# Performance work log

Measured on AMD Instinct MI355X. Metric: run time of the kernel, lower is better.

Reference implementation:

```python
import jax, jax.numpy as jnp
import numpy as np

C_IN, C_OUT = 64, 32
SD, RFF = 2, 16
RF = 0.05          # receptive_field percentile
TEMP = 1.0
EPS = 1e-8
RFF_STD = 6.0


def setup_inputs() -> dict:
    key = jax.random.key(0)
    ks = jax.random.split(key, 10)
    B_, T, V, Q = 2, 4, 2048, 512
    x = jax.random.normal(ks[0], (B_, T, V, C_IN), dtype=jnp.float32)
    pos = jax.random.uniform(ks[1], (V, SD), dtype=jnp.float32)
    query_pos = jax.random.uniform(ks[2], (Q, SD), dtype=jnp.float32)
    s = 1.0 / np.sqrt(C_IN)
    W_lin = jax.random.uniform(ks[3], (C_IN, C_IN), minval=-s, maxval=s, dtype=jnp.float32)
    b_lin = jax.random.uniform(ks[4], (C_IN,), minval=-s, maxval=s, dtype=jnp.float32)
    Bmat = RFF_STD * jax.random.normal(ks[5], (SD, RFF), dtype=jnp.float32)
    s1 = 1.0 / np.sqrt(32)
    W1 = jax.random.uniform(ks[6], (32, 32), minval=-s1, maxval=s1, dtype=jnp.float32)
    b1 = jax.random.uniform(ks[7], (32,), minval=-s1, maxval=s1, dtype=jnp.float32)
    W2 = jax.random.uniform(ks[8], (C_IN * C_OUT, 32), minval=-s1, maxval=s1, dtype=jnp.float32)
    sf = np.sqrt(3.0 / C_IN)
    filt = jax.random.uniform(ks[9], (C_IN * C_OUT,), minval=-sf, maxval=sf, dtype=jnp.float32)
    bias = jnp.zeros((C_OUT,), dtype=jnp.float32)
    return {"x": x, "pos": pos, "query_pos": query_pos, "W_lin": W_lin, "b_lin": b_lin,
            "Bmat": Bmat, "W1": W1, "b1": b1, "W2": W2, "filt": filt, "bias": bias}


def reference(x, pos, query_pos, W_lin, b_lin, Bmat, W1, b1, W2, filt, bias):
    # pairwise periodic displacement / squared distance
    dist = query_pos[:, None, :] - pos[None, :, :]            # (Q, V, 2)
    dist = (dist + 0.5) % 1.0 - 0.5                           # periodic wrap
    edist = jnp.sum(dist ** 2, axis=-1)                       # (Q, V)
    # quantile threshold -> max neighbourhood size (eager, data-dependent like torch)
    thr = jnp.quantile(edist, RF, axis=-1, keepdims=True)     # linear interpolation, as torch
    K = int(jnp.max(jnp.sum(edist <= thr, axis=-1)))
    _, ind = jax.lax.top_k(-edist, K)                         # (Q, K) nearest neighbours
    # gather per-query neighbour displacements / distances
    d_g = jnp.take_along_axis(dist, ind[..., None], axis=1)   # (Q, K, 2)
    e_g = jnp.take_along_axis(edist, ind, axis=1)[..., None]  # (Q, K, 1)
    e_g = e_g - jnp.min(e_g, axis=-2, keepdims=True)
    e_g = e_g / (jnp.max(e_g, axis=-2, keepdims=True) + EPS)
    k_dist = jax.nn.softmax(-e_g / TEMP, axis=-2)             # (Q, K, 1)
    # random Fourier features + kernel MLP
    proj = 2.0 * jnp.pi * (d_g @ Bmat)                        # (Q, K, 16)
    kfeat = jnp.concatenate([jnp.sin(proj), jnp.cos(proj)], axis=-1)  # (Q, K, 32)
    h = jax.nn.gelu(kfeat @ W1.T + b1, approximate=False)
    ker = (h @ W2.T + filt) * k_dist                          # (Q, K, C_IN*C_OUT)
    ker = ker.reshape(ker.shape[0], ker.shape[1], C_IN, C_OUT)
    # point-wise linear on features, then gather + contract
    xl = x @ W_lin.T + b_lin                                  # (B, T, V, C_IN)
    xg = xl[:, :, ind, :]                                     # (B, T, Q, K, C_IN)
    return jnp.einsum('qvcd,btqvc->btqd', ker, xg) + bias     # (B, T, Q, C_OUT)
```

## Files before the change

### kernel.cpp

```cpp
#include <hip/hip_runtime.h>

#define K_SEL 103
typedef unsigned long long ull_t;
typedef _Float16 f16x8 __attribute__((ext_vector_type(8)));
typedef float f32x4 __attribute__((ext_vector_type(4)));

__global__ __launch_bounds__(256, 4) void k12(const float* __restrict__ pos,
                                              const float* __restrict__ qpos,
                                              const float* __restrict__ Bmat,
                                              const float* __restrict__ W1,
                                              const float* __restrict__ b1,
                                              _Float16* __restrict__ Hh,
                                              int* __restrict__ indg,
                                              float* __restrict__ invtot,
                                              const float* __restrict__ x,
                                              const float* __restrict__ W,
                                              const float* __restrict__ b,
                                              _Float16* __restrict__ xlh,
                                              const float* __restrict__ W2,
                                              const float* __restrict__ filt,
                                              _Float16* __restrict__ W2th) {
    __shared__ __align__(16) unsigned char smem[30848];
    const int tid = threadIdx.x;
    const int bid = blockIdx.x;
    const int lane = tid & 63;
    const int wid = tid >> 6;

    if (bid >= 512) {
        const int bb = bid - 512;
        float* Wt = (float*)smem;
        if (tid < 132) {
            int t = bb * 132 + tid;
            int d = t & 31;
            int e = t >> 5;
            int c = e & 63;
            int j = e >> 6;
            float v = (j < 32) ? W2[(c * 32 + d) * 32 + j] : filt[c * 32 + d];
            W2th[d * 2112 + e] = (_Float16)v;
        }
        for (int t = tid; t < 4096; t += 256)
            Wt[(t & 63) * 64 + (t >> 6)] = W[t];
        __syncthreads();
        const int i = tid & 63;
        const int sub = tid >> 6;
        const float bi = b[i];
        #pragma unroll
        for (int rr = 0; rr < 2; ++rr) {
            const int r0 = bb * 32 + rr * 16 + sub * 4;
            float acc0 = bi, acc1 = bi, acc2 = bi, acc3 = bi;
            const float* xr = x + (size_t)r0 * 64;
            #pragma unroll 4
            for (int jj = 0; jj < 16; ++jj) {
                float4 v0 = *(const float4*)(xr + 0 * 64 + jj * 4);
                float4 v1 = *(const float4*)(xr + 1 * 64 + jj * 4);
                float4 v2 = *(const float4*)(xr + 2 * 64 + jj * 4);
                float4 v3 = *(const float4*)(xr + 3 * 64 + jj * 4);
                float w0 = Wt[(jj * 4 + 0) * 64 + i];
                float w1 = Wt[(jj * 4 + 1) * 64 + i];
                float w2 = Wt[(jj * 4 + 2) * 64 + i];
                float w3 = Wt[(jj * 4 + 3) * 64 + i];
                acc0 += v0.x * w0 + v0.y * w1 + v0.z * w2 + v0.w * w3;
                acc1 += v1.x * w0 + v1.y * w1 + v1.z * w2 + v1.w * w3;
                acc2 += v2.x * w0 + v2.y * w1 + v2.z * w2 + v2.w * w3;
                acc3 += v3.x * w0 + v3.y * w1 + v3.z * w2 + v3.w * w3;
            }
            xlh[(size_t)(r0 + 0) * 64 + i] = (_Float16)acc0;
            xlh[(size_t)(r0 + 1) * 64 + i] = (_Float16)acc1;
            xlh[(size_t)(r0 + 2) * 64 + i] = (_Float16)acc2;
            xlh[(size_t)(r0 + 3) * 64 + i] = (_Float16)acc3;
        }
        return;
    }

    const int q = bid;
    unsigned* ebits   = (unsigned*)(smem);
    unsigned* hist    = (unsigned*)(smem + 8192);
    _Float16* Hs      = (_Float16*)(smem + 8192);
    float*    W1s     = (float*)(smem + 24576);
    float*    b1s     = (float*)(smem + 28672);
    float*    Bm      = (float*)(smem + 28800);
    int*      sel_v   = (int*)(smem + 28928);
    float*    sel_e   = (float*)(smem + 29344);
    ull_t*    bnd     = (ull_t*)(smem + 29760);
    int*      counters= (int*)(smem + 30784);
    int*      info    = (int*)(smem + 30792);
    float*    wred    = (float*)(smem + 30800);
    float*    emax_s  = (float*)(smem + 30816);
    unsigned* wscan   = (unsigned*)(smem + 30824);

    for (int t = tid; t < 1024; t += 256) W1s[t] = W1[t];
    if (tid < 32) { b1s[tid] = b1[tid]; Bm[tid] = Bmat[tid]; }
    if (tid < 2)  counters[tid] = 0;
    for (int t = tid; t < 1024; t += 256) ((uint4*)hist)[t] = make_uint4(0, 0, 0, 0);
    const float qp0 = qpos[q * 2 + 0];
    const float qp1 = qpos[q * 2 + 1];
    __syncthreads();

    float lmin = 1e30f;
    for (int v = tid; v < 2048; v += 256) {
        float2 p = ((const float2*)pos)[v];
        float d0 = qp0 - p.x;
        float d1 = qp1 - p.y;
        d0 += 0.5f; d0 -= floorf(d0); d0 -= 0.5f;
        d1 += 0.5f; d1 -= floorf(d1); d1 -= 0.5f;
        float e = d0 * d0 + d1 * d1;
        ebits[v] = __float_as_uint(e);
        lmin = fminf(lmin, e);
        int bb2 = (int)(e * 8192.0f); bb2 = (bb2 > 4095) ? 4095 : bb2;
        atomicAdd(&hist[bb2], 1u);
    }
    #pragma unroll
    for (int off = 32; off > 0; off >>= 1)
        lmin = fminf(lmin, __shfl_xor(lmin, off, 64));
    if (lane == 0) wred[wid] = lmin;
    __syncthreads();
    const float e_min = fminf(fminf(wred[0], wred[1]), fminf(wred[2], wred[3]));

    unsigned lsum = 0;
    #pragma unroll
    for (int i = 0; i < 16; ++i) lsum += hist[tid * 16 + i];
    unsigned vq = lsum;
    #pragma unroll
    for (int off = 1; off < 64; off <<= 1) {
        unsigned n = __shfl_up(vq, off, 64);
        if (lane >= off) vq += n;
    }
    if (lane == 63) wscan[wid] = vq;
    __syncthreads();
    unsigned base = 0;
    for (int w2 = 0; w2 < wid; ++w2) base += wscan[w2];
    unsigned cum = base + vq - lsum;
    #pragma unroll
    for (int i = 0; i < 16; ++i) {
        unsigned cnt = hist[tid * 16 + i];
        if (cum <= 102u && 102u < cum + cnt) { info[0] = tid * 16 + i; info[1] = (int)cum; }
        cum += cnt;
    }
    __syncthreads();
    const int Bstar = info[0];
    const int L = info[1];
    const int need = K_SEL - L;

    {
        f16x8 z = {0, 0, 0, 0, 0, 0, 0, 0};
        for (int t = tid; t < 768; t += 256) ((f16x8*)Hs)[t] = z;
    }
    for (int v = tid; v < 2048; v += 256) {
        unsigned bb2 = ebits[v];
        float e = __uint_as_float(bb2);
        int bin = (int)(e * 8192.0f); bin = (bin > 4095) ? 4095 : bin;
        if (bin < Bstar) {
            int s2 = atomicAdd(&counters[0], 1);
            sel_v[s2] = v; sel_e[s2] = e;
        } else if (bin == Bstar) {
            int s2 = atomicAdd(&counters[1], 1);
            if (s2 < 128) bnd[s2] = (((ull_t)bb2) << 32) | (unsigned)v;
        }
    }
    __syncthreads();
    if (tid == 0) {
        int nb = counters[1]; if (nb > 128) nb = 128;
        for (int i = 1; i < nb; ++i) {
            ull_t key = bnd[i]; int j2 = i - 1;
            while (j2 >= 0 && bnd[j2] > key) { bnd[j2 + 1] = bnd[j2]; --j2; }
            bnd[j2 + 1] = key;
        }
        for (int i = 0; i < need; ++i) {
            sel_v[L + i] = (int)(unsigned)(bnd[i] & 0xffffffffull);
            sel_e[L + i] = __uint_as_float((unsigned)(bnd[i] >> 32));
        }
        emax_s[0] = __uint_as_float((unsigned)(bnd[need - 1] >> 32));
    }
    __syncthreads();

    const float denom = (emax_s[0] - e_min) + 1e-8f;
    float w = 0.0f;
    if (tid < K_SEL) {
        w = __expf(-(sel_e[tid] - e_min) / denom);
        sel_e[tid] = w;
    }
    float sw = w;
    #pragma unroll
    for (int off = 32; off > 0; off >>= 1)
        sw += __shfl_xor(sw, off, 64);
    if (lane == 0) wred[wid] = sw;
    __syncthreads();
    if (tid == 0)
        invtot[q] = 1.0f / (wred[0] + wred[1] + wred[2] + wred[3]);

    if (tid < 2 * K_SEL) {
        const int k = tid >> 1;
        const int io = (tid & 1) * 16;
        const int v = sel_v[k];
        const float wk = sel_e[k];
        float2 p = ((const float2*)pos)[v];
        float d0 = qp0 - p.x;
        float d1 = qp1 - p.y;
        d0 += 0.5f; d0 -= floorf(d0); d0 -= 0.5f;
        d1 += 0.5f; d1 -= floorf(d1); d1 -= 0.5f;
        float kf[32];
        #pragma unroll
        for (int f = 0; f < 16; ++f) {
            float t = d0 * Bm[f] + d1 * Bm[16 + f];
            float r = t - rintf(t);
            kf[f]      = __builtin_amdgcn_sinf(r);
            kf[16 + f] = __builtin_amdgcn_cosf(r);
        }
        #pragma unroll 4
        for (int i = io; i < io + 16; ++i) {
            float pre = b1s[i];
            #pragma unroll
            for (int jf = 0; jf < 32; ++jf) pre += kf[jf] * W1s[i * 32 + jf];
            float g = 0.5f * pre * (1.0f + erff(pre * 0.70710678118654752f));
            Hs[i * 128 + k] = (_Float16)(g * wk);
        }
        if (io == 0) {
            Hs[32 * 128 + k] = (_Float16)wk;
            indg[q * K_SEL + k] = v;
        }
    }
    __syncthreads();
    {
        _Float16* hq = Hh + (size_t)q * 6144;
        for (int t = tid; t < 768; t += 256)
            ((f16x8*)hq)[t] = ((const f16x8*)Hs)[t];
    }
}

__global__ __launch_bounds__(256, 4) void k3_main(const _Float16* __restrict__ xlh,
                                                  const _Float16* __restrict__ Hh,
                                                  const int* __restrict__ indg,
                                                  const _Float16* __restrict__ W2th,
                                                  const float* __restrict__ bias,
                                                  const float* __restrict__ invtot,
                                                  float* __restrict__ out) {
    const int bid = blockIdx.x;
    const int q = bid >> 1;
    const int tid = threadIdx.x;
    const int lane = tid & 63;
    const int wv = tid >> 6;
    const int n0 = lane & 15;
    const int quad = lane >> 4;

    __shared__ __align__(16) unsigned char smem[36608];
    _Float16* Xg = (_Float16*)smem;
    _Float16* Zh = Xg;
    float* red = (float*)(smem + 35072);
    int* ind_s = (int*)(smem + 36096);

    const _Float16* hq = Hh + (size_t)q * 6144;
    f16x8 afr[4][3];
    #pragma unroll
    for (int ks = 0; ks < 4; ++ks)
        #pragma unroll
        for (int r = 0; r < 3; ++r)
            afr[ks][r] = *(const f16x8*)(hq + (r * 16 + n0) * 128 + ks * 32 + quad * 8);
    const float it = invtot[q];
    if (tid < 128) {
        int kk = (tid < K_SEL) ? tid : tid - K_SEL;
        ind_s[tid] = indg[q * K_SEL + kk];
    }
    __syncthreads();

    int g_bt[8], g_k[8], g_oct[8];
    #pragma unroll
    for (int i = 0; i < 8; ++i) {
        int t = tid + i * 256;
        g_bt[i] = t >> 10;
        int r = t & 1023;
        g_k[i] = r >> 3;
        g_oct[i] = r & 7;
    }
    const int bt0A = (bid & 1) * 4;
    const int bt0B = bt0A + 2;

    {
        f16x8 v[8];
        #pragma unroll
        for (int i = 0; i < 8; ++i)
            v[i] = *(const f16x8*)(xlh + ((size_t)(bt0A + g_bt[i]) * 2048 + ind_s[g_k[i]]) * 64 + g_oct[i] * 8);
        #pragma unroll
        for (int i = 0; i < 8; ++i) {
            int base = g_bt[i] * 8768 + g_oct[i] * 1096 + g_k[i];
            #pragma unroll
            for (int jj = 0; jj < 8; ++jj) Xg[base + 136 * jj] = v[i][jj];
        }
    }
    __syncthreads();

    f16x8 vB[8];
    #pragma unroll
    for (int i = 0; i < 8; ++i)
        vB[i] = *(const f16x8*)(xlh + ((size_t)(bt0B + g_bt[i]) * 2048 + ind_s[g_k[i]]) * 64 + g_oct[i] * 8);

    #pragma unroll
    for (int pass = 0; pass < 2; ++pass) {
        const int bt0 = pass ? bt0B : bt0A;
        if (pass) {
            #pragma unroll
            for (int i = 0; i < 8; ++i) {
                int base = g_bt[i] * 8768 + g_oct[i] * 1096 + g_k[i];
                #pragma unroll
                for (int jj = 0; jj < 8; ++jj) Xg[base + 136 * jj] = vB[i][jj];
            }
            __syncthreads();
        }

        f32x4 Dz[3][2];
        #pragma unroll
        for (int r = 0; r < 3; ++r)
            #pragma unroll
            for (int c = 0; c < 2; ++c) Dz[r][c] = (f32x4){0.f, 0.f, 0.f, 0.f};
        #pragma unroll
        for (int ks = 0; ks < 4; ++ks) {
            const int kbase = ks * 32 + quad * 8;
            #pragma unroll
            for (int ctl = 0; ctl < 2; ++ctl) {
                const int ct = wv * 2 + ctl;
                const int bt = ct >> 2;
                const int c = (ct & 3) * 16 + n0;
                f16x8 bfr = *(const f16x8*)(&Xg[bt * 8768 + c * 136 + ((c >> 3) << 3) + kbase]);
                #pragma unroll
                for (int r = 0; r < 3; ++r)
                    Dz[r][ctl] = __builtin_amdgcn_mfma_f32_16x16x32_f16(afr[ks][r], bfr, Dz[r][ctl], 0, 0, 0);
            }
        }
        __syncthreads();

        #pragma unroll
        for (int ctl = 0; ctl < 2; ++ctl) {
            const int ct = wv * 2 + ctl;
            const int bt = ct >> 2;
            const int c = (ct & 3) * 16 + n0;
            #pragma unroll
            for (int r = 0; r < 3; ++r)
                #pragma unroll
                for (int reg = 0; reg < 4; ++reg) {
                    int j = r * 16 + quad * 4 + reg;
                    if (j < 33) Zh[bt * 2112 + j * 64 + c] = (_Float16)Dz[r][ctl][reg];
                }
        }
        __syncthreads();

        f32x4 D2[2][2];
        #pragma unroll
        for (int p = 0; p < 2; ++p)
            #pragma unroll
            for (int dt = 0; dt < 2; ++dt) D2[p][dt] = (f32x4){0.f, 0.f, 0.f, 0.f};
        int p = 0;
        #pragma unroll 2
        for (int s = wv; s < 66; s += 4) {
            const int e0 = s * 32 + quad * 8;
            f16x8 afr2 = {0, 0, 0, 0, 0, 0, 0, 0};
            if (n0 < 2) afr2 = *(const f16x8*)(&Zh[n0 * 2112 + e0]);
            #pragma unroll
            for (int dt = 0; dt < 2; ++dt) {
                f16x8 bfr = *(const f16x8*)(W2th + (size_t)(dt * 16 + n0) * 2112 + e0);
                D2[p][dt] = __builtin_amdgcn_mfma_f32_16x16x32_f16(afr2, bfr, D2[p][dt], 0, 0, 0);
            }
            p ^= 1;
        }
        #pragma unroll
        for (int dt = 0; dt < 2; ++dt)
            D2[0][dt] = D2[0][dt] + D2[1][dt];

        if (quad == 0) {
            red[(wv * 4 + 0) * 16 + n0] = D2[0][0][0];
            red[(wv * 4 + 1) * 16 + n0] = D2[0][0][1];
            red[(wv * 4 + 2) * 16 + n0] = D2[0][1][0];
            red[(wv * 4 + 3) * 16 + n0] = D2[0][1][1];
        }
        __syncthreads();
        if (tid < 64) {
            const int bt = tid >> 5;
            const int d = tid & 31;
            const int dt = d >> 4;
            const int dn = d & 15;
            float s = 0.0f;
            #pragma unroll
            for (int w2 = 0; w2 < 4; ++w2)
                s += red[(w2 * 4 + dt * 2 + bt) * 16 + dn];
            out[((size_t)(bt0 + bt) * 512 + q) * 32 + d] = bias[d] + it * s;
        }
    }
}

extern "C" void kernel_launch(void* const* d_in, const int* in_sizes, int n_in,
                              void* d_out, int out_size, void* d_ws, size_t ws_size,
                              hipStream_t stream) {
    const float* x     = (const float*)d_in[0];
    const float* pos   = (const float*)d_in[1];
    const float* qpos  = (const float*)d_in[2];
    const float* W_lin = (const float*)d_in[3];
    const float* b_lin = (const float*)d_in[4];
    const float* Bmat  = (const float*)d_in[5];
    const float* W1    = (const float*)d_in[6];
    const float* b1    = (const float*)d_in[7];
    const float* W2    = (const float*)d_in[8];
    const float* filt  = (const float*)d_in[9];
    const float* bias  = (const float*)d_in[10];
    float* out = (float*)d_out;

    float* ws = (float*)d_ws;
    _Float16* xlh    = (_Float16*)ws;
    _Float16* Hh     = (_Float16*)(ws + 524288);
    int*      indg   = (int*)(ws + 2097152);
    _Float16* W2th   = (_Float16*)(ws + 2150144);
    float*    invtot = ws + 2183936;

    k12<<<1024, 256, 0, stream>>>(pos, qpos, Bmat, W1, b1, Hh, indg, invtot,
                                  x, W_lin, b_lin, xlh, W2, filt, W2th);
    k3_main<<<1024, 256, 0, stream>>>(xlh, Hh, indg, W2th, bias, invtot, out);
}
```

Measured before the change: 134.0 us.

## Split k3_main into four blocks per query with paired-neighbor LDS stores

k3_main now launches 2048 blocks, so each block handles two batch-time slices instead of four. Both gathers are issued up front, and each 32-bit LDS store writes two neighbors' fp16 values. The second slice's staging and its Z write-back overlap with the first slice's results, and the smaller LDS footprint allows launch bounds of 5 blocks per SM. In exchange, each block reloads the H fragment and the W2 weights, doubling that redundant traffic per query.

```diff
diff --git a/kernel.cpp b/kernel.cpp
--- a/kernel.cpp
+++ b/kernel.cpp
@@ -3,6 +3,7 @@
 #define K_SEL 103
 typedef unsigned long long ull_t;
 typedef _Float16 f16x8 __attribute__((ext_vector_type(8)));
+typedef short s16x8 __attribute__((ext_vector_type(8)));
 typedef float f32x4 __attribute__((ext_vector_type(4)));
 
 __global__ __launch_bounds__(256, 4) void k12(const float* __restrict__ pos,
@@ -227,7 +228,7 @@
     }
 }
 
-__global__ __launch_bounds__(256, 4) void k3_main(const _Float16* __restrict__ xlh,
+__global__ __launch_bounds__(256, 5) void k3_main(const _Float16* __restrict__ xlh,
                                                   const _Float16* __restrict__ Hh,
                                                   const int* __restrict__ indg,
                                                   const _Float16* __restrict__ W2th,
@@ -235,18 +236,19 @@
                                                   const float* __restrict__ invtot,
                                                   float* __restrict__ out) {
     const int bid = blockIdx.x;
-    const int q = bid >> 1;
+    const int q = bid >> 2;
+    const int pr = bid & 3;
     const int tid = threadIdx.x;
     const int lane = tid & 63;
     const int wv = tid >> 6;
     const int n0 = lane & 15;
     const int quad = lane >> 4;
 
-    __shared__ __align__(16) unsigned char smem[36608];
-    _Float16* Xg = (_Float16*)smem;
-    _Float16* Zh = Xg;
-    float* red = (float*)(smem + 35072);
-    int* ind_s = (int*)(smem + 36096);
+    __shared__ __align__(16) unsigned char smem[26464];
+    _Float16* Xg   = (_Float16*)smem;
+    _Float16* Zh   = (_Float16*)(smem + 17504);
+    int*      ind_s= (int*)(smem + 25952);
+    float*    red  = (float*)smem;
 
     const _Float16* hq = Hh + (size_t)q * 6144;
     f16x8 afr[4][3];
@@ -262,126 +264,134 @@
     }
     __syncthreads();
 
-    int g_bt[8], g_k[8], g_oct[8];
-    #pragma unroll
-    for (int i = 0; i < 8; ++i) {
-        int t = tid + i * 256;
-        g_bt[i] = t >> 10;
-        int r = t & 1023;
-        g_k[i] = r >> 3;
-        g_oct[i] = r & 7;
-    }
-    const int bt0A = (bid & 1) * 4;
-    const int bt0B = bt0A + 2;
-
-    {
-        f16x8 v[8];
-        #pragma unroll
-        for (int i = 0; i < 8; ++i)
-            v[i] = *(const f16x8*)(xlh + ((size_t)(bt0A + g_bt[i]) * 2048 + ind_s[g_k[i]]) * 64 + g_oct[i] * 8);
-        #pragma unroll
-        for (int i = 0; i < 8; ++i) {
-            int base = g_bt[i] * 8768 + g_oct[i] * 1096 + g_k[i];
-            #pragma unroll
-            for (int jj = 0; jj < 8; ++jj) Xg[base + 136 * jj] = v[i][jj];
-        }
-    }
-    __syncthreads();
-
-    f16x8 vB[8];
-    #pragma unroll
-    for (int i = 0; i < 8; ++i)
-        vB[i] = *(const f16x8*)(xlh + ((size_t)(bt0B + g_bt[i]) * 2048 + ind_s[g_k[i]]) * 64 + g_oct[i] * 8);
-
-    #pragma unroll
-    for (int pass = 0; pass < 2; ++pass) {
-        const int bt0 = pass ? bt0B : bt0A;
-        if (pass) {
-            #pragma unroll
-            for (int i = 0; i < 8; ++i) {
-                int base = g_bt[i] * 8768 + g_oct[i] * 1096 + g_k[i];
-                #pragma unroll
-                for (int jj = 0; jj < 8; ++jj) Xg[base + 136 * jj] = vB[i][jj];
-            }
-            __syncthreads();
-        }
-
-        f32x4 Dz[3][2];
+    int g_k2[2], g_oct[2];
+    #pragma unroll
+    for (int i = 0; i < 2; ++i) {
+        int s = tid + i * 256;
+        g_k2[i] = s >> 3;
+        g_oct[i] = s & 7;
+    }
+    const int btA = pr * 2, btB = pr * 2 + 1;
+
+    f16x8 vA[2][2], vB[2][2];
+    #pragma unroll
+    for (int i = 0; i < 2; ++i) {
+        const int ka = ind_s[2 * g_k2[i]];
+        const int kb = ind_s[2 * g_k2[i] + 1];
+        vA[i][0] = *(const f16x8*)(xlh + ((size_t)btA * 2048 + ka) * 64 + g_oct[i] * 8);
+        vA[i][1] = *(const f16x8*)(xlh + ((size_t)btA * 2048 + kb) * 64 + g_oct[i] * 8);
+        vB[i][0] = *(const f16x8*)(xlh + ((size_t)btB * 2048 + ka) * 64 + g_oct[i] * 8);
+        vB[i][1] = *(const f16x8*)(xlh + ((size_t)btB * 2048 + kb) * 64 + g_oct[i] * 8);
+    }
+
+    #pragma unroll
+    for (int i = 0; i < 2; ++i) {
+        s16x8 lo = __builtin_bit_cast(s16x8, vA[i][0]);
+        s16x8 hi = __builtin_bit_cast(s16x8, vA[i][1]);
+        int base = g_oct[i] * 1096 + 2 * g_k2[i];
+        #pragma unroll
+        for (int cc = 0; cc < 8; ++cc) {
+            unsigned u = ((unsigned)(unsigned short)lo[cc]) |
+                         (((unsigned)(unsigned short)hi[cc]) << 16);
+            *(unsigned*)(&Xg[base + 136 * cc]) = u;
+        }
+    }
+    __syncthreads();
+
+    f32x4 DzA[3];
+    #pragma unroll
+    for (int r = 0; r < 3; ++r) DzA[r] = (f32x4){0.f, 0.f, 0.f, 0.f};
+    const int cA = wv * 16 + n0;
+    const int cswz = cA * 136 + ((cA >> 3) << 3);
+    #pragma unroll
+    for (int ks = 0; ks < 4; ++ks) {
+        f16x8 bfr = *(const f16x8*)(&Xg[cswz + ks * 32 + quad * 8]);
         #pragma unroll
         for (int r = 0; r < 3; ++r)
-            #pragma unroll
-            for (int c = 0; c < 2; ++c) Dz[r][c] = (f32x4){0.f, 0.f, 0.f, 0.f};
-        #pragma unroll
-        for (int ks = 0; ks < 4; ++ks) {
-            const int kbase = ks * 32 + quad * 8;
-            #pragma unroll
-            for (int ctl = 0; ctl < 2; ++ctl) {
-                const int ct = wv * 2 + ctl;
-                const int bt = ct >> 2;
-                const int c = (ct & 3) * 16 + n0;
-                f16x8 bfr = *(const f16x8*)(&Xg[bt * 8768 + c * 136 + ((c >> 3) << 3) + kbase]);
-                #pragma unroll
-                for (int r = 0; r < 3; ++r)
-                    Dz[r][ctl] = __builtin_amdgcn_mfma_f32_16x16x32_f16(afr[ks][r], bfr, Dz[r][ctl], 0, 0, 0);
-            }
-        }
-        __syncthreads();
-
-        #pragma unroll
-        for (int ctl = 0; ctl < 2; ++ctl) {
-            const int ct = wv * 2 + ctl;
-            const int bt = ct >> 2;
-            const int c = (ct & 3) * 16 + n0;
-            #pragma unroll
-            for (int r = 0; r < 3; ++r)
-                #pragma unroll
-                for (int reg = 0; reg < 4; ++reg) {
-                    int j = r * 16 + quad * 4 + reg;
-                    if (j < 33) Zh[bt * 2112 + j * 64 + c] = (_Float16)Dz[r][ctl][reg];
-                }
-        }
-        __syncthreads();
-
-        f32x4 D2[2][2];
-        #pragma unroll
-        for (int p = 0; p < 2; ++p)
-            #pragma unroll
-            for (int dt = 0; dt < 2; ++dt) D2[p][dt] = (f32x4){0.f, 0.f, 0.f, 0.f};
-        int p = 0;
-        #pragma unroll 2
-        for (int s = wv; s < 66; s += 4) {
-            const int e0 = s * 32 + quad * 8;
-            f16x8 afr2 = {0, 0, 0, 0, 0, 0, 0, 0};
-            if (n0 < 2) afr2 = *(const f16x8*)(&Zh[n0 * 2112 + e0]);
-            #pragma unroll
-            for (int dt = 0; dt < 2; ++dt) {
-                f16x8 bfr = *(const f16x8*)(W2th + (size_t)(dt * 16 + n0) * 2112 + e0);
-                D2[p][dt] = __builtin_amdgcn_mfma_f32_16x16x32_f16(afr2, bfr, D2[p][dt], 0, 0, 0);
-            }
-            p ^= 1;
-        }
-        #pragma unroll
-        for (int dt = 0; dt < 2; ++dt)
-            D2[0][dt] = D2[0][dt] + D2[1][dt];
-
-        if (quad == 0) {
-            red[(wv * 4 + 0) * 16 + n0] = D2[0][0][0];
-            red[(wv * 4 + 1) * 16 + n0] = D2[0][0][1];
-            red[(wv * 4 + 2) * 16 + n0] = D2[0][1][0];
-            red[(wv * 4 + 3) * 16 + n0] = D2[0][1][1];
-        }
-        __syncthreads();
-        if (tid < 64) {
-            const int bt = tid >> 5;
-            const int d = tid & 31;
-            const int dt = d >> 4;
-            const int dn = d & 15;
-            float s = 0.0f;
-            #pragma unroll
-            for (int w2 = 0; w2 < 4; ++w2)
-                s += red[(w2 * 4 + dt * 2 + bt) * 16 + dn];
-            out[((size_t)(bt0 + bt) * 512 + q) * 32 + d] = bias[d] + it * s;
-        }
+            DzA[r] = __builtin_amdgcn_mfma_f32_16x16x32_f16(afr[ks][r], bfr, DzA[r], 0, 0, 0);
+    }
+    __syncthreads();
+
+    #pragma unroll
+    for (int i = 0; i < 2; ++i) {
+        s16x8 lo = __builtin_bit_cast(s16x8, vB[i][0]);
+        s16x8 hi = __builtin_bit_cast(s16x8, vB[i][1]);
+        int base = g_oct[i] * 1096 + 2 * g_k2[i];
+        #pragma unroll
+        for (int cc = 0; cc < 8; ++cc) {
+            unsigned u = ((unsigned)(unsigned short)lo[cc]) |
+                         (((unsigned)(unsigned short)hi[cc]) << 16);
+            *(unsigned*)(&Xg[base + 136 * cc]) = u;
+        }
+    }
+    #pragma unroll
+    for (int r = 0; r < 3; ++r)
+        #pragma unroll
+        for (int reg = 0; reg < 4; ++reg) {
+            int j = r * 16 + quad * 4 + reg;
+            if (j < 33) Zh[j * 64 + cA] = (_Float16)DzA[r][reg];
+        }
+    __syncthreads();
+
+    f32x4 DzB[3];
+    #pragma unroll
+    for (int r = 0; r < 3; ++r) DzB[r] = (f32x4){0.f, 0.f, 0.f, 0.f};
+    #pragma unroll
+    for (int ks = 0; ks < 4; ++ks) {
+        f16x8 bfr = *(const f16x8*)(&Xg[cswz + ks * 32 + quad * 8]);
+        #pragma unroll
+        for (int r = 0; r < 3; ++r)
+            DzB[r] = __builtin_amdgcn_mfma_f32_16x16x32_f16(afr[ks][r], bfr, DzB[r], 0, 0, 0);
+    }
+    #pragma unroll
+    for (int r = 0; r < 3; ++r)
+        #pragma unroll
+        for (int reg = 0; reg < 4; ++reg) {
+            int j = r * 16 + quad * 4 + reg;
+            if (j < 33) Zh[2112 + j * 64 + cA] = (_Float16)DzB[r][reg];
+        }
+    __syncthreads();
+
+    f32x4 D2[2][2];
+    #pragma unroll
+    for (int p = 0; p < 2; ++p)
+        #pragma unroll
+        for (int dt = 0; dt < 2; ++dt) D2[p][dt] = (f32x4){0.f, 0.f, 0.f, 0.f};
+    int p = 0;
+    #pragma unroll 2
+    for (int s = wv; s < 66; s += 4) {
+        const int e0 = s * 32 + quad * 8;
+        f16x8 afr2 = {0, 0, 0, 0, 0, 0, 0, 0};
+        if (n0 < 2) afr2 = *(const f16x8*)(&Zh[n0 * 2112 + e0]);
+        #pragma unroll
+        for (int dt = 0; dt < 2; ++dt) {
+            f16x8 bfr = *(const f16x8*)(W2th + (size_t)(dt * 16 + n0) * 2112 + e0);
+            D2[p][dt] = __builtin_amdgcn_mfma_f32_16x16x32_f16(afr2, bfr, D2[p][dt], 0, 0, 0);
+        }
+        p ^= 1;
+    }
+    #pragma unroll
+    for (int dt = 0; dt < 2; ++dt)
+        D2[0][dt] = D2[0][dt] + D2[1][dt];
+    __syncthreads();
+
+    if (quad == 0) {
+        red[(wv * 4 + 0) * 16 + n0] = D2[0][0][0];
+        red[(wv * 4 + 1) * 16 + n0] = D2[0][0][1];
+        red[(wv * 4 + 2) * 16 + n0] = D2[0][1][0];
+        red[(wv * 4 + 3) * 16 + n0] = D2[0][1][1];
+    }
+    __syncthreads();
+    if (tid < 64) {
+        const int btl = tid >> 5;
+        const int d = tid & 31;
+        const int dt = d >> 4;
+        const int dn = d & 15;
+        float s = 0.0f;
+        #pragma unroll
+        for (int w2 = 0; w2 < 4; ++w2)
+            s += red[(w2 * 4 + dt * 2 + btl) * 16 + dn];
+        out[((size_t)(pr * 2 + btl) * 512 + q) * 32 + d] = bias[d] + it * s;
     }
 }
 
@@ -410,5 +420,5 @@
 
     k12<<<1024, 256, 0, stream>>>(pos, qpos, Bmat, W1, b1, Hh, indg, invtot,
                                   x, W_lin, b_lin, xlh, W2, filt, W2th);
-    k3_main<<<1024, 256, 0, stream>>>(xlh, Hh, indg, W2th, bias, invtot, out);
+    k3_main<<<2048, 256, 0, stream>>>(xlh, Hh, indg, W2th, bias, invtot, out);
 }
```

Result: slower. 138.8 us (+3.6%).

## Split per-query kernel-feature work across two blocks and compact selection deterministically

Applied to the files above, without the earlier changes.

Each query is now handled by two blocks in k12. Both redundantly run the distance/histogram selection, and each computes and writes half of the neighbour kernel-MLP rows (56 vs 47). Selected neighbours are compacted with a wave prefix scan instead of atomics, which makes the order identical across the two blocks. The linear-projection blocks process twice the rows, with padded shared memory (stride 65) to avoid bank conflicts, and launch bounds rise to 5. k3_main prefetches the first W2th fragments before the barrier. The split trades duplicated selection work for more parallelism on the sin/cos/GELU stage.

```diff
diff --git a/kernel.cpp b/kernel.cpp
--- a/kernel.cpp
+++ b/kernel.cpp
@@ -5,7 +5,7 @@
 typedef _Float16 f16x8 __attribute__((ext_vector_type(8)));
 typedef float f32x4 __attribute__((ext_vector_type(4)));
 
-__global__ __launch_bounds__(256, 4) void k12(const float* __restrict__ pos,
+__global__ __launch_bounds__(256, 5) void k12(const float* __restrict__ pos,
                                               const float* __restrict__ qpos,
                                               const float* __restrict__ Bmat,
                                               const float* __restrict__ W1,
@@ -26,11 +26,11 @@
     const int lane = tid & 63;
     const int wid = tid >> 6;
 
-    if (bid >= 512) {
-        const int bb = bid - 512;
+    if (bid >= 1024) {
+        const int bb = bid - 1024;
         float* Wt = (float*)smem;
-        if (tid < 132) {
-            int t = bb * 132 + tid;
+        for (int t2 = tid; t2 < 264; t2 += 256) {
+            int t = bb * 264 + t2;
             int d = t & 31;
             int e = t >> 5;
             int c = e & 63;
@@ -39,14 +39,14 @@
             W2th[d * 2112 + e] = (_Float16)v;
         }
         for (int t = tid; t < 4096; t += 256)
-            Wt[(t & 63) * 64 + (t >> 6)] = W[t];
+            Wt[(t & 63) * 65 + (t >> 6)] = W[t];
         __syncthreads();
         const int i = tid & 63;
         const int sub = tid >> 6;
         const float bi = b[i];
         #pragma unroll
-        for (int rr = 0; rr < 2; ++rr) {
-            const int r0 = bb * 32 + rr * 16 + sub * 4;
+        for (int rr = 0; rr < 4; ++rr) {
+            const int r0 = bb * 64 + rr * 16 + sub * 4;
             float acc0 = bi, acc1 = bi, acc2 = bi, acc3 = bi;
             const float* xr = x + (size_t)r0 * 64;
             #pragma unroll 4
@@ -55,10 +55,10 @@
                 float4 v1 = *(const float4*)(xr + 1 * 64 + jj * 4);
                 float4 v2 = *(const float4*)(xr + 2 * 64 + jj * 4);
                 float4 v3 = *(const float4*)(xr + 3 * 64 + jj * 4);
-                float w0 = Wt[(jj * 4 + 0) * 64 + i];
-                float w1 = Wt[(jj * 4 + 1) * 64 + i];
-                float w2 = Wt[(jj * 4 + 2) * 64 + i];
-                float w3 = Wt[(jj * 4 + 3) * 64 + i];
+                float w0 = Wt[(jj * 4 + 0) * 65 + i];
+                float w1 = Wt[(jj * 4 + 1) * 65 + i];
+                float w2 = Wt[(jj * 4 + 2) * 65 + i];
+                float w3 = Wt[(jj * 4 + 3) * 65 + i];
                 acc0 += v0.x * w0 + v0.y * w1 + v0.z * w2 + v0.w * w3;
                 acc1 += v1.x * w0 + v1.y * w1 + v1.z * w2 + v1.w * w3;
                 acc2 += v2.x * w0 + v2.y * w1 + v2.z * w2 + v2.w * w3;
@@ -72,7 +72,8 @@
         return;
     }
 
-    const int q = bid;
+    const int q = bid >> 1;
+    const int par = bid & 1;
     unsigned* ebits   = (unsigned*)(smem);
     unsigned* hist    = (unsigned*)(smem + 8192);
     _Float16* Hs      = (_Float16*)(smem + 8192);
@@ -145,18 +146,32 @@
         f16x8 z = {0, 0, 0, 0, 0, 0, 0, 0};
         for (int t = tid; t < 768; t += 256) ((f16x8*)Hs)[t] = z;
     }
-    for (int v = tid; v < 2048; v += 256) {
+
+    int myv[8]; float mye[8]; int mycnt = 0;
+    #pragma unroll
+    for (int i2 = 0; i2 < 8; ++i2) {
+        int v = tid * 8 + i2;
         unsigned bb2 = ebits[v];
         float e = __uint_as_float(bb2);
         int bin = (int)(e * 8192.0f); bin = (bin > 4095) ? 4095 : bin;
-        if (bin < Bstar) {
-            int s2 = atomicAdd(&counters[0], 1);
-            sel_v[s2] = v; sel_e[s2] = e;
-        } else if (bin == Bstar) {
+        if (bin < Bstar) { myv[mycnt] = v; mye[mycnt] = e; ++mycnt; }
+        else if (bin == Bstar) {
             int s2 = atomicAdd(&counters[1], 1);
             if (s2 < 128) bnd[s2] = (((ull_t)bb2) << 32) | (unsigned)v;
         }
     }
+    unsigned vq2 = (unsigned)mycnt;
+    #pragma unroll
+    for (int off = 1; off < 64; off <<= 1) {
+        unsigned n = __shfl_up(vq2, off, 64);
+        if (lane >= off) vq2 += n;
+    }
+    if (lane == 63) wscan[wid] = vq2;
+    __syncthreads();
+    unsigned base2 = 0;
+    for (int w2 = 0; w2 < wid; ++w2) base2 += wscan[w2];
+    int P = (int)(base2 + vq2) - mycnt;
+    for (int j2 = 0; j2 < mycnt; ++j2) { sel_v[P + j2] = myv[j2]; sel_e[P + j2] = mye[j2]; }
     __syncthreads();
     if (tid == 0) {
         int nb = counters[1]; if (nb > 128) nb = 128;
@@ -188,8 +203,10 @@
     if (tid == 0)
         invtot[q] = 1.0f / (wred[0] + wred[1] + wred[2] + wred[3]);
 
-    if (tid < 2 * K_SEL) {
-        const int k = tid >> 1;
+    const int kbase = par * 56;
+    const int kcnt  = par ? (K_SEL - 56) : 56;
+    if (tid < 2 * kcnt) {
+        const int k = kbase + (tid >> 1);
         const int io = (tid & 1) * 16;
         const int v = sel_v[k];
         const float wk = sel_e[k];
@@ -222,8 +239,19 @@
     __syncthreads();
     {
         _Float16* hq = Hh + (size_t)q * 6144;
-        for (int t = tid; t < 768; t += 256)
-            ((f16x8*)hq)[t] = ((const f16x8*)Hs)[t];
+        if (par == 0) {
+            for (int t = tid; t < 336; t += 256) {
+                int row = t / 7, c8 = t - row * 7;
+                int off = row * 128 + c8 * 8;
+                *(f16x8*)(hq + off) = *(const f16x8*)(&Hs[off]);
+            }
+        } else {
+            for (int t = tid; t < 432; t += 256) {
+                int row = t / 9, c8 = t - row * 9;
+                int off = row * 128 + 56 + c8 * 8;
+                *(f16x8*)(hq + off) = *(const f16x8*)(&Hs[off]);
+            }
+        }
     }
 }
 
@@ -256,6 +284,9 @@
         for (int r = 0; r < 3; ++r)
             afr[ks][r] = *(const f16x8*)(hq + (r * 16 + n0) * 128 + ks * 32 + quad * 8);
     const float it = invtot[q];
+    const int e0f = wv * 32 + quad * 8;
+    f16x8 pf0 = *(const f16x8*)(W2th + (size_t)(0 * 16 + n0) * 2112 + e0f);
+    f16x8 pf1 = *(const f16x8*)(W2th + (size_t)(1 * 16 + n0) * 2112 + e0f);
     if (tid < 128) {
         int kk = (tid < K_SEL) ? tid : tid - K_SEL;
         ind_s[tid] = indg[q * K_SEL + kk];
@@ -347,9 +378,15 @@
         for (int p = 0; p < 2; ++p)
             #pragma unroll
             for (int dt = 0; dt < 2; ++dt) D2[p][dt] = (f32x4){0.f, 0.f, 0.f, 0.f};
-        int p = 0;
+        {
+            f16x8 afr2 = {0, 0, 0, 0, 0, 0, 0, 0};
+            if (n0 < 2) afr2 = *(const f16x8*)(&Zh[n0 * 2112 + e0f]);
+            D2[0][0] = __builtin_amdgcn_mfma_f32_16x16x32_f16(afr2, pf0, D2[0][0], 0, 0, 0);
+            D2[0][1] = __builtin_amdgcn_mfma_f32_16x16x32_f16(afr2, pf1, D2[0][1], 0, 0, 0);
+        }
+        int p = 1;
         #pragma unroll 2
-        for (int s = wv; s < 66; s += 4) {
+        for (int s = wv + 4; s < 66; s += 4) {
             const int e0 = s * 32 + quad * 8;
             f16x8 afr2 = {0, 0, 0, 0, 0, 0, 0, 0};
             if (n0 < 2) afr2 = *(const f16x8*)(&Zh[n0 * 2112 + e0]);
@@ -408,7 +445,7 @@
     _Float16* W2th   = (_Float16*)(ws + 2150144);
     float*    invtot = ws + 2183936;
 
-    k12<<<1024, 256, 0, stream>>>(pos, qpos, Bmat, W1, b1, Hh, indg, invtot,
+    k12<<<1280, 256, 0, stream>>>(pos, qpos, Bmat, W1, b1, Hh, indg, invtot,
                                   x, W_lin, b_lin, xlh, W2, filt, W2th);
     k3_main<<<1024, 256, 0, stream>>>(xlh, Hh, indg, W2th, bias, invtot, out);
 }
```

Result: slower. 179.3 us (+33.8%).

## Pipeline per-bt gathers in k3 and batch the W2 contraction over four bt

Applied to the files above, without the earlier changes.

k3_main now gathers one bt slice at a time, using a half-size smem buffer, and prefetches the next slice while MFMAs run on the current one. The stage-1 results for all four bt values are staged in smem, so the W2th contraction runs once with four active MFMA rows instead of twice with two. This halves the W2th global reads per block and prefetches the first W2th fragments early. It also pads the transposed W_lin smem tile in k12 to stride 65 to avoid bank conflicts, at the cost of more barriers per block and slightly more smem for the Z buffer.

```diff
diff --git a/kernel.cpp b/kernel.cpp
--- a/kernel.cpp
+++ b/kernel.cpp
@@ -39,7 +39,7 @@
             W2th[d * 2112 + e] = (_Float16)v;
         }
         for (int t = tid; t < 4096; t += 256)
-            Wt[(t & 63) * 64 + (t >> 6)] = W[t];
+            Wt[(t & 63) * 65 + (t >> 6)] = W[t];
         __syncthreads();
         const int i = tid & 63;
         const int sub = tid >> 6;
@@ -55,10 +55,10 @@
                 float4 v1 = *(const float4*)(xr + 1 * 64 + jj * 4);
                 float4 v2 = *(const float4*)(xr + 2 * 64 + jj * 4);
                 float4 v3 = *(const float4*)(xr + 3 * 64 + jj * 4);
-                float w0 = Wt[(jj * 4 + 0) * 64 + i];
-                float w1 = Wt[(jj * 4 + 1) * 64 + i];
-                float w2 = Wt[(jj * 4 + 2) * 64 + i];
-                float w3 = Wt[(jj * 4 + 3) * 64 + i];
+                float w0 = Wt[(jj * 4 + 0) * 65 + i];
+                float w1 = Wt[(jj * 4 + 1) * 65 + i];
+                float w2 = Wt[(jj * 4 + 2) * 65 + i];
+                float w3 = Wt[(jj * 4 + 3) * 65 + i];
                 acc0 += v0.x * w0 + v0.y * w1 + v0.z * w2 + v0.w * w3;
                 acc1 += v1.x * w0 + v1.y * w1 + v1.z * w2 + v1.w * w3;
                 acc2 += v2.x * w0 + v2.y * w1 + v2.z * w2 + v2.w * w3;
@@ -236,17 +236,18 @@
                                                   float* __restrict__ out) {
     const int bid = blockIdx.x;
     const int q = bid >> 1;
+    const int bt0 = (bid & 1) * 4;
     const int tid = threadIdx.x;
     const int lane = tid & 63;
     const int wv = tid >> 6;
     const int n0 = lane & 15;
     const int quad = lane >> 4;
 
-    __shared__ __align__(16) unsigned char smem[36608];
-    _Float16* Xg = (_Float16*)smem;
-    _Float16* Zh = Xg;
-    float* red = (float*)(smem + 35072);
-    int* ind_s = (int*)(smem + 36096);
+    __shared__ __align__(16) unsigned char smem[34944];
+    _Float16* Xg  = (_Float16*)smem;
+    _Float16* Zh4 = (_Float16*)(smem + 17536);
+    int* ind_s    = (int*)(smem + 34432);
+    float* red    = (float*)smem;
 
     const _Float16* hq = Hh + (size_t)q * 6144;
     f16x8 afr[4][3];
@@ -256,132 +257,124 @@
         for (int r = 0; r < 3; ++r)
             afr[ks][r] = *(const f16x8*)(hq + (r * 16 + n0) * 128 + ks * 32 + quad * 8);
     const float it = invtot[q];
+    const int e0f = wv * 32 + quad * 8;
+    f16x8 pf0 = *(const f16x8*)(W2th + (size_t)(0 * 16 + n0) * 2112 + e0f);
+    f16x8 pf1 = *(const f16x8*)(W2th + (size_t)(1 * 16 + n0) * 2112 + e0f);
     if (tid < 128) {
         int kk = (tid < K_SEL) ? tid : tid - K_SEL;
         ind_s[tid] = indg[q * K_SEL + kk];
     }
     __syncthreads();
 
-    int g_bt[8], g_k[8], g_oct[8];
-    #pragma unroll
-    for (int i = 0; i < 8; ++i) {
+    int g_k[4], g_oct[4];
+    #pragma unroll
+    for (int i = 0; i < 4; ++i) {
         int t = tid + i * 256;
-        g_bt[i] = t >> 10;
-        int r = t & 1023;
-        g_k[i] = r >> 3;
-        g_oct[i] = r & 7;
-    }
-    const int bt0A = (bid & 1) * 4;
-    const int bt0B = bt0A + 2;
+        g_k[i] = t >> 3;
+        g_oct[i] = t & 7;
+    }
 
     {
-        f16x8 v[8];
-        #pragma unroll
-        for (int i = 0; i < 8; ++i)
-            v[i] = *(const f16x8*)(xlh + ((size_t)(bt0A + g_bt[i]) * 2048 + ind_s[g_k[i]]) * 64 + g_oct[i] * 8);
-        #pragma unroll
-        for (int i = 0; i < 8; ++i) {
-            int base = g_bt[i] * 8768 + g_oct[i] * 1096 + g_k[i];
-            #pragma unroll
-            for (int jj = 0; jj < 8; ++jj) Xg[base + 136 * jj] = v[i][jj];
-        }
-    }
-    __syncthreads();
-
-    f16x8 vB[8];
-    #pragma unroll
-    for (int i = 0; i < 8; ++i)
-        vB[i] = *(const f16x8*)(xlh + ((size_t)(bt0B + g_bt[i]) * 2048 + ind_s[g_k[i]]) * 64 + g_oct[i] * 8);
-
-    #pragma unroll
-    for (int pass = 0; pass < 2; ++pass) {
-        const int bt0 = pass ? bt0B : bt0A;
-        if (pass) {
-            #pragma unroll
-            for (int i = 0; i < 8; ++i) {
-                int base = g_bt[i] * 8768 + g_oct[i] * 1096 + g_k[i];
+        f16x8 v0[4];
+        #pragma unroll
+        for (int i = 0; i < 4; ++i)
+            v0[i] = *(const f16x8*)(xlh + ((size_t)bt0 * 2048 + ind_s[g_k[i]]) * 64 + g_oct[i] * 8);
+        #pragma unroll
+        for (int i = 0; i < 4; ++i) {
+            int base = g_oct[i] * 1096 + g_k[i];
+            #pragma unroll
+            for (int jj = 0; jj < 8; ++jj) Xg[base + 136 * jj] = v0[i][jj];
+        }
+    }
+    __syncthreads();
+
+    const int cA = wv * 16 + n0;
+    const int cswz = cA * 136 + ((cA >> 3) << 3);
+
+    #pragma unroll
+    for (int p = 0; p < 4; ++p) {
+        f16x8 vn[4];
+        if (p < 3) {
+            #pragma unroll
+            for (int i = 0; i < 4; ++i)
+                vn[i] = *(const f16x8*)(xlh + ((size_t)(bt0 + p + 1) * 2048 + ind_s[g_k[i]]) * 64 + g_oct[i] * 8);
+        }
+        f32x4 Dz[3];
+        #pragma unroll
+        for (int r = 0; r < 3; ++r) Dz[r] = (f32x4){0.f, 0.f, 0.f, 0.f};
+        #pragma unroll
+        for (int ks = 0; ks < 4; ++ks) {
+            f16x8 bfr = *(const f16x8*)(&Xg[cswz + ks * 32 + quad * 8]);
+            #pragma unroll
+            for (int r = 0; r < 3; ++r)
+                Dz[r] = __builtin_amdgcn_mfma_f32_16x16x32_f16(afr[ks][r], bfr, Dz[r], 0, 0, 0);
+        }
+        __syncthreads();
+        #pragma unroll
+        for (int r = 0; r < 3; ++r)
+            #pragma unroll
+            for (int reg = 0; reg < 4; ++reg) {
+                int j = r * 16 + quad * 4 + reg;
+                if (j < 33) Zh4[p * 2112 + j * 64 + cA] = (_Float16)Dz[r][reg];
+            }
+        if (p < 3) {
+            #pragma unroll
+            for (int i = 0; i < 4; ++i) {
+                int base = g_oct[i] * 1096 + g_k[i];
                 #pragma unroll
-                for (int jj = 0; jj < 8; ++jj) Xg[base + 136 * jj] = vB[i][jj];
+                for (int jj = 0; jj < 8; ++jj) Xg[base + 136 * jj] = vn[i][jj];
             }
             __syncthreads();
         }
-
-        f32x4 Dz[3][2];
-        #pragma unroll
-        for (int r = 0; r < 3; ++r)
-            #pragma unroll
-            for (int c = 0; c < 2; ++c) Dz[r][c] = (f32x4){0.f, 0.f, 0.f, 0.f};
-        #pragma unroll
-        for (int ks = 0; ks < 4; ++ks) {
-            const int kbase = ks * 32 + quad * 8;
-            #pragma unroll
-            for (int ctl = 0; ctl < 2; ++ctl) {
-                const int ct = wv * 2 + ctl;
-                const int bt = ct >> 2;
-                const int c = (ct & 3) * 16 + n0;
-                f16x8 bfr = *(const f16x8*)(&Xg[bt * 8768 + c * 136 + ((c >> 3) << 3) + kbase]);
-                #pragma unroll
-                for (int r = 0; r < 3; ++r)
-                    Dz[r][ctl] = __builtin_amdgcn_mfma_f32_16x16x32_f16(afr[ks][r], bfr, Dz[r][ctl], 0, 0, 0);
-            }
-        }
-        __syncthreads();
-
-        #pragma unroll
-        for (int ctl = 0; ctl < 2; ++ctl) {
-            const int ct = wv * 2 + ctl;
-            const int bt = ct >> 2;
-            const int c = (ct & 3) * 16 + n0;
-            #pragma unroll
-            for (int r = 0; r < 3; ++r)
-                #pragma unroll
-                for (int reg = 0; reg < 4; ++reg) {
-                    int j = r * 16 + quad * 4 + reg;
-                    if (j < 33) Zh[bt * 2112 + j * 64 + c] = (_Float16)Dz[r][ctl][reg];
-                }
-        }
-        __syncthreads();
-
-        f32x4 D2[2][2];
-        #pragma unroll
-        for (int p = 0; p < 2; ++p)
-            #pragma unroll
-            for (int dt = 0; dt < 2; ++dt) D2[p][dt] = (f32x4){0.f, 0.f, 0.f, 0.f};
-        int p = 0;
-        #pragma unroll 2
-        for (int s = wv; s < 66; s += 4) {
-            const int e0 = s * 32 + quad * 8;
-            f16x8 afr2 = {0, 0, 0, 0, 0, 0, 0, 0};
-            if (n0 < 2) afr2 = *(const f16x8*)(&Zh[n0 * 2112 + e0]);
-            #pragma unroll
-            for (int dt = 0; dt < 2; ++dt) {
-                f16x8 bfr = *(const f16x8*)(W2th + (size_t)(dt * 16 + n0) * 2112 + e0);
-                D2[p][dt] = __builtin_amdgcn_mfma_f32_16x16x32_f16(afr2, bfr, D2[p][dt], 0, 0, 0);
-            }
-            p ^= 1;
-        }
+    }
+    __syncthreads();
+
+    f32x4 D2[2][2];
+    #pragma unroll
+    for (int pp = 0; pp < 2; ++pp)
+        #pragma unroll
+        for (int dt = 0; dt < 2; ++dt) D2[pp][dt] = (f32x4){0.f, 0.f, 0.f, 0.f};
+    {
+        f16x8 a2 = {0, 0, 0, 0, 0, 0, 0, 0};
+        if (n0 < 4) a2 = *(const f16x8*)(&Zh4[n0 * 2112 + e0f]);
+        D2[0][0] = __builtin_amdgcn_mfma_f32_16x16x32_f16(a2, pf0, D2[0][0], 0, 0, 0);
+        D2[0][1] = __builtin_amdgcn_mfma_f32_16x16x32_f16(a2, pf1, D2[0][1], 0, 0, 0);
+    }
+    int pp = 1;
+    #pragma unroll 2
+    for (int s = wv + 4; s < 66; s += 4) {
+        const int e0 = s * 32 + quad * 8;
+        f16x8 a2 = {0, 0, 0, 0, 0, 0, 0, 0};
+        if (n0 < 4) a2 = *(const f16x8*)(&Zh4[n0 * 2112 + e0]);
+        #pragma unroll
+        for (int dt = 0; dt < 2; ++dt) {
+            f16x8 bfr = *(const f16x8*)(W2th + (size_t)(dt * 16 + n0) * 2112 + e0);
+            D2[pp][dt] = __builtin_amdgcn_mfma_f32_16x16x32_f16(a2, bfr, D2[pp][dt], 0, 0, 0);
+        }
+        pp ^= 1;
+    }
+    #pragma unroll
+    for (int dt = 0; dt < 2; ++dt)
+        D2[0][dt] = D2[0][dt] + D2[1][dt];
+
+    if (quad == 0) {
         #pragma unroll
         for (int dt = 0; dt < 2; ++dt)
-            D2[0][dt] = D2[0][dt] + D2[1][dt];
-
-        if (quad == 0) {
-            red[(wv * 4 + 0) * 16 + n0] = D2[0][0][0];
-            red[(wv * 4 + 1) * 16 + n0] = D2[0][0][1];
-            red[(wv * 4 + 2) * 16 + n0] = D2[0][1][0];
-            red[(wv * 4 + 3) * 16 + n0] = D2[0][1][1];
-        }
-        __syncthreads();
-        if (tid < 64) {
-            const int bt = tid >> 5;
-            const int d = tid & 31;
-            const int dt = d >> 4;
-            const int dn = d & 15;
-            float s = 0.0f;
-            #pragma unroll
-            for (int w2 = 0; w2 < 4; ++w2)
-                s += red[(w2 * 4 + dt * 2 + bt) * 16 + dn];
-            out[((size_t)(bt0 + bt) * 512 + q) * 32 + d] = bias[d] + it * s;
-        }
+            #pragma unroll
+            for (int reg = 0; reg < 4; ++reg)
+                red[((wv * 2 + dt) * 4 + reg) * 16 + n0] = D2[0][dt][reg];
+    }
+    __syncthreads();
+    if (tid < 128) {
+        const int bt = tid >> 5;
+        const int d = tid & 31;
+        const int dt = d >> 4;
+        const int dn = d & 15;
+        float s = 0.0f;
+        #pragma unroll
+        for (int w2 = 0; w2 < 4; ++w2)
+            s += red[((w2 * 2 + dt) * 4 + bt) * 16 + dn];
+        out[((size_t)(bt0 + bt) * 512 + q) * 32 + d] = bias[d] + it * s;
     }
 }
 
```

After: 121.2 us. 1.11x faster.
